# Kernel optimization log

Hardware: AMD Instinct MI355X
Metric: run time of the kernel (lower is better)

## Reference

```python
import jax, jax.numpy as jnp
import numpy as np

N_SP = 32  # number of superpixels, hardcoded in the original module


def setup_inputs() -> dict:
    key = jax.random.key(0)
    k1, k2 = jax.random.split(key)
    b, c, h, w = 16, 64, 512, 512
    features = jax.random.normal(k1, (b, c, h, w), dtype=jnp.float32)
    superpixel_indices = jax.random.randint(k2, (b, h, w), 0, N_SP, dtype=jnp.int32)
    return {"features": features, "superpixel_indices": superpixel_indices}


def reference(features, superpixel_indices):
    b, c, h, w = features.shape
    # [b, h*w, c]
    feats = jnp.transpose(features, (0, 2, 3, 1)).reshape(b * h * w, c)
    # offset segment ids so all batches reduce in one segment_sum pass
    ids = (superpixel_indices.reshape(b, h * w)
           + (jnp.arange(b, dtype=superpixel_indices.dtype)[:, None] * N_SP)).reshape(-1)
    sums = jax.ops.segment_sum(feats, ids, num_segments=b * N_SP)          # [b*N, c]
    counts = jax.ops.segment_sum(jnp.ones((b * h * w,), feats.dtype), ids,
                                 num_segments=b * N_SP)                     # [b*N]
    # mean per superpixel; empty superpixels stay zero (matches torch init)
    sp = jnp.where(counts[:, None] > 0,
                   sums / jnp.maximum(counts[:, None], 1.0),
                   0.0).reshape(b, N_SP, c)
    # pairwise: sim[i,j] = 1 - 0.5 * ||sp_i - sp_j||^2  (N=32, tiny)
    diff = sp[:, :, None, :] - sp[:, None, :, :]        # [b, N, N, c]
    sim = 1.0 - 0.5 * jnp.sum(diff * diff, axis=-1)     # [b, N, N]
    return sp, sim
```

## Files before the change

### kernel.cpp

```cpp
#include <hip/hip_runtime.h>

#define NSP 32
#define BB  16
#define CC  64
#define HH  512
#define WW  512
#define HW  (HH * WW)

#define CHUNK  8192
#define BLOCK  256
#define NCHUNK (HW / CHUNK)

#define CNT_CHUNK 16384

__global__ __launch_bounds__(BLOCK) void sp_accum(const float* __restrict__ feats,
                                                  const int*   __restrict__ spidx,
                                                  float*       __restrict__ sums )
{
    __shared__ unsigned char s_idx[CHUNK];
    __shared__ float2 s_priv[BLOCK][NSP + 1];
    __shared__ float2 s_part[8][NSP];

    const int tid  = threadIdx.x;
    const int b    = blockIdx.y;
    const int pix0 = blockIdx.x * CHUNK;

    const int4* ip = (const int4*)(spidx + (size_t)b * HW + pix0);
    uchar4* sip = (uchar4*)s_idx;
    for (int i = tid; i < CHUNK / 4; i += BLOCK) {
        int4 v = ip[i];
        sip[i] = make_uchar4((unsigned char)(v.x & 31), (unsigned char)(v.y & 31),
                             (unsigned char)(v.z & 31), (unsigned char)(v.w & 31));
    }
#pragma unroll
    for (int sp = 0; sp < NSP; ++sp) s_priv[tid][sp] = make_float2(0.f, 0.f);
    __syncthreads();

    const int bin = tid & 31;
    const int grp = tid >> 5;

    for (int cp = 0; cp < CC; cp += 2) {
        const float4* f0 = (const float4*)(feats + ((size_t)b * CC + cp)     * HW + pix0);
        const float4* f1 = (const float4*)(feats + ((size_t)b * CC + cp + 1) * HW + pix0);
        float2* row = s_priv[tid];

#pragma unroll
        for (int k = 0; k < CHUNK / 4 / BLOCK; ++k) {
            const int i = k * BLOCK + tid;
            float4 a = f0[i];
            float4 c = f1[i];
            uchar4 u = sip[i];
            float2 t;
            t = row[u.x]; t.x += a.x; t.y += c.x; row[u.x] = t;
            t = row[u.y]; t.x += a.y; t.y += c.y; row[u.y] = t;
            t = row[u.z]; t.x += a.z; t.y += c.z; row[u.z] = t;
            t = row[u.w]; t.x += a.w; t.y += c.w; row[u.w] = t;
        }
        __syncthreads();

        float2 acc = make_float2(0.f, 0.f);
#pragma unroll
        for (int m = 0; m < BLOCK / 8; ++m) {
            float2 v = s_priv[grp + m * 8][bin];
            acc.x += v.x; acc.y += v.y;
        }
        s_part[grp][bin] = acc;
        __syncthreads();

        if (cp + 2 < CC) {
#pragma unroll
            for (int sp = 0; sp < NSP; ++sp) s_priv[tid][sp] = make_float2(0.f, 0.f);
        }
        if (tid < NSP) {
            float2 r = s_part[0][tid];
#pragma unroll
            for (int g2 = 1; g2 < 8; ++g2) { r.x += s_part[g2][tid].x; r.y += s_part[g2][tid].y; }
            atomicAdd(&sums[((size_t)b * CC + cp)     * NSP + tid], r.x);
            atomicAdd(&sums[((size_t)b * CC + cp + 1) * NSP + tid], r.y);
        }
        __syncthreads();
    }
}

__global__ __launch_bounds__(BLOCK) void sp_count(const int* __restrict__ spidx,
                                                  float*     __restrict__ counts )
{
    __shared__ int s_cnt[BLOCK][NSP + 1];
    __shared__ int s_tot[NSP];
    const int tid  = threadIdx.x;
    const int b    = blockIdx.y;
    const int pix0 = blockIdx.x * CNT_CHUNK;

#pragma unroll
    for (int sp = 0; sp < NSP; ++sp) s_cnt[tid][sp] = 0;
    if (tid < NSP) s_tot[tid] = 0;
    __syncthreads();

    const int4* ip = (const int4*)(spidx + (size_t)b * HW + pix0);
    int* row = s_cnt[tid];
    for (int i = tid; i < CNT_CHUNK / 4; i += BLOCK) {
        int4 v = ip[i];
        row[v.x & 31]++;
        row[v.y & 31]++;
        row[v.z & 31]++;
        row[v.w & 31]++;
    }
    __syncthreads();

    const int bin = tid & 31, grp = tid >> 5;
    int acc = 0;
#pragma unroll
    for (int m = 0; m < BLOCK / 8; ++m) acc += s_cnt[grp + m * 8][bin];
    atomicAdd(&s_tot[bin], acc);
    __syncthreads();

    if (tid < NSP) atomicAdd(&counts[b * NSP + tid], (float)s_tot[tid]);
}

__global__ __launch_bounds__(BLOCK) void sp_finalize(const float* __restrict__ sums,
                                                     const float* __restrict__ counts,
                                                     float*       __restrict__ out)
{
    __shared__ float s_sp[NSP][CC + 1];
    const int b   = blockIdx.x;
    const int tid = threadIdx.x;

    for (int i = tid; i < NSP * CC; i += BLOCK) {
        int sp = i >> 6, c = i & 63;
        float cnt = counts[b * NSP + sp];
        float s   = sums[((size_t)b * CC + c) * NSP + sp];
        float v   = (cnt > 0.0f) ? (s / cnt) : 0.0f;
        s_sp[sp][c] = v;
        out[(size_t)b * NSP * CC + (size_t)sp * CC + c] = v;
    }
    __syncthreads();

    for (int p = tid; p < NSP * NSP; p += BLOCK) {
        int i = p >> 5, j = p & 31;
        float acc = 0.0f;
#pragma unroll
        for (int c = 0; c < CC; ++c) {
            float d = s_sp[i][c] - s_sp[j][c];
            acc = fmaf(d, d, acc);
        }
        out[(size_t)BB * NSP * CC + (size_t)b * NSP * NSP + p] = 1.0f - 0.5f * acc;
    }
}

extern "C" void kernel_launch(void* const* d_in, const int* in_sizes, int n_in,
                              void* d_out, int out_size, void* d_ws, size_t ws_size,
                              hipStream_t stream)
{
    const float* feats = (const float*)d_in[0];
    const int*   spidx = (const int*)d_in[1];
    float*       out   = (float*)d_out;

    float* sums   = (float*)d_ws;
    float* counts = sums + (size_t)BB * CC * NSP;

    hipMemsetAsync(d_ws, 0, ((size_t)BB * CC * NSP + (size_t)BB * NSP) * sizeof(float), stream);

    dim3 g1(NCHUNK, BB);
    sp_accum<<<g1, BLOCK, 0, stream>>>(feats, spidx, sums);

    dim3 g2(HW / CNT_CHUNK, BB);
    sp_count<<<g2, BLOCK, 0, stream>>>(spidx, counts);

    sp_finalize<<<BB, BLOCK, 0, stream>>>(sums, counts, out);
}
```

Baseline: 224.6 us.

## Fuse count kernel into accumulation and prefetch next channel pair into registers

Removes the separate sp_count kernel and computes per-superpixel counts inside sp_accum from the already-staged index tile, saving one launch and a second read of the index array. The feature loads for the next channel pair are issued into registers before the reduction and barrier phases, so global memory latency overlaps with the shared-memory reduction. __syncthreads is replaced by an inline-asm barrier that waits only on LDS counters, which lets the prefetched global loads stay in flight across barriers. This raises register pressure (16 float4 values held per thread) and depends on the hand-written barrier being correct.

```diff
diff --git a/kernel.cpp b/kernel.cpp
--- a/kernel.cpp
+++ b/kernel.cpp
@@ -3,118 +3,124 @@
 #define NSP 32
 #define BB  16
 #define CC  64
-#define HH  512
-#define WW  512
-#define HW  (HH * WW)
+#define HW  (512 * 512)
 
+#define BLOCK  256
 #define CHUNK  8192
-#define BLOCK  256
 #define NCHUNK (HW / CHUNK)
+#define KIT    (CHUNK / 4 / BLOCK)
 
-#define CNT_CHUNK 16384
+#define BAR() asm volatile("s_waitcnt lgkmcnt(0)\n\ts_barrier" ::: "memory")
 
 __global__ __launch_bounds__(BLOCK) void sp_accum(const float* __restrict__ feats,
                                                   const int*   __restrict__ spidx,
-                                                  float*       __restrict__ sums )
+                                                  float*       __restrict__ sums  ,
+                                                  float*       __restrict__ counts)
 {
-    __shared__ unsigned char s_idx[CHUNK];
+    __shared__ uchar4 s_idx[CHUNK / 4];
     __shared__ float2 s_priv[BLOCK][NSP + 1];
     __shared__ float2 s_part[8][NSP];
 
     const int tid  = threadIdx.x;
     const int b    = blockIdx.y;
     const int pix0 = blockIdx.x * CHUNK;
+    const int bin  = tid & 31;
+    const int grp  = tid >> 5;
 
     const int4* ip = (const int4*)(spidx + (size_t)b * HW + pix0);
-    uchar4* sip = (uchar4*)s_idx;
-    for (int i = tid; i < CHUNK / 4; i += BLOCK) {
+#pragma unroll
+    for (int n = 0; n < (CHUNK / 4) / BLOCK; ++n) {
+        const int i = n * BLOCK + tid;
         int4 v = ip[i];
-        sip[i] = make_uchar4((unsigned char)(v.x & 31), (unsigned char)(v.y & 31),
-                             (unsigned char)(v.z & 31), (unsigned char)(v.w & 31));
+        s_idx[i] = make_uchar4((unsigned char)(v.x & 31), (unsigned char)(v.y & 31),
+                               (unsigned char)(v.z & 31), (unsigned char)(v.w & 31));
     }
 #pragma unroll
     for (int sp = 0; sp < NSP; ++sp) s_priv[tid][sp] = make_float2(0.f, 0.f);
-    __syncthreads();
 
-    const int bin = tid & 31;
-    const int grp = tid >> 5;
+    const float* fb = feats + (size_t)b * CC * HW + pix0;
+    float4 pre[KIT][2];
+#pragma unroll
+    for (int k = 0; k < KIT; ++k) {
+        pre[k][0] = ((const float4*)fb)[k * BLOCK + tid];
+        pre[k][1] = ((const float4*)(fb + (size_t)HW))[k * BLOCK + tid];
+    }
 
-    for (int cp = 0; cp < CC; cp += 2) {
-        const float4* f0 = (const float4*)(feats + ((size_t)b * CC + cp)     * HW + pix0);
-        const float4* f1 = (const float4*)(feats + ((size_t)b * CC + cp + 1) * HW + pix0);
-        float2* row = s_priv[tid];
+    BAR();
 
+    {
+        float* rowf = (float*)&s_priv[tid][0];
 #pragma unroll
-        for (int k = 0; k < CHUNK / 4 / BLOCK; ++k) {
-            const int i = k * BLOCK + tid;
-            float4 a = f0[i];
-            float4 c = f1[i];
-            uchar4 u = sip[i];
+        for (int k = 0; k < KIT; ++k) {
+            uchar4 u = s_idx[k * BLOCK + tid];
+            rowf[u.x * 2] += 1.f;
+            rowf[u.y * 2] += 1.f;
+            rowf[u.z * 2] += 1.f;
+            rowf[u.w * 2] += 1.f;
+        }
+    }
+    BAR();
+    {
+        float a = 0.f;
+#pragma unroll
+        for (int m = 0; m < BLOCK / 8; ++m) a += s_priv[grp + m * 8][bin].x;
+        s_part[grp][bin].x = a;
+    }
+    BAR();
+    if (tid < NSP) {
+        float r = 0.f;
+#pragma unroll
+        for (int g = 0; g < 8; ++g) r += s_part[g][tid].x;
+        atomicAdd(&counts[b * NSP + tid], r);
+    }
+#pragma unroll
+    for (int sp = 0; sp < NSP; ++sp) s_priv[tid][sp] = make_float2(0.f, 0.f);
+    BAR();
+
+    float2* row = s_priv[tid];
+    for (int cp = 0; cp < CC / 2; ++cp) {
+#pragma unroll
+        for (int k = 0; k < KIT; ++k) {
+            uchar4 u = s_idx[k * BLOCK + tid];
+            float4 a = pre[k][0], c = pre[k][1];
             float2 t;
             t = row[u.x]; t.x += a.x; t.y += c.x; row[u.x] = t;
             t = row[u.y]; t.x += a.y; t.y += c.y; row[u.y] = t;
             t = row[u.z]; t.x += a.z; t.y += c.z; row[u.z] = t;
             t = row[u.w]; t.x += a.w; t.y += c.w; row[u.w] = t;
         }
-        __syncthreads();
-
-        float2 acc = make_float2(0.f, 0.f);
+        if (cp + 1 < CC / 2) {
+            const float* g0 = fb + (size_t)(2 * cp + 2) * HW;
 #pragma unroll
-        for (int m = 0; m < BLOCK / 8; ++m) {
-            float2 v = s_priv[grp + m * 8][bin];
-            acc.x += v.x; acc.y += v.y;
+            for (int k = 0; k < KIT; ++k) {
+                pre[k][0] = ((const float4*)g0)[k * BLOCK + tid];
+                pre[k][1] = ((const float4*)(g0 + (size_t)HW))[k * BLOCK + tid];
+            }
         }
-        s_part[grp][bin] = acc;
-        __syncthreads();
-
-        if (cp + 2 < CC) {
+        BAR();
+        {
+            float2 acc = make_float2(0.f, 0.f);
 #pragma unroll
-            for (int sp = 0; sp < NSP; ++sp) s_priv[tid][sp] = make_float2(0.f, 0.f);
+            for (int m = 0; m < BLOCK / 8; ++m) {
+                float2 v = s_priv[grp + m * 8][bin];
+                acc.x += v.x; acc.y += v.y;
+            }
+            s_part[grp][bin] = acc;
+        }
+        BAR();
+        if (cp + 1 < CC / 2) {
+#pragma unroll
+            for (int sp = 0; sp < NSP; ++sp) row[sp] = make_float2(0.f, 0.f);
         }
         if (tid < NSP) {
             float2 r = s_part[0][tid];
 #pragma unroll
-            for (int g2 = 1; g2 < 8; ++g2) { r.x += s_part[g2][tid].x; r.y += s_part[g2][tid].y; }
-            atomicAdd(&sums[((size_t)b * CC + cp)     * NSP + tid], r.x);
-            atomicAdd(&sums[((size_t)b * CC + cp + 1) * NSP + tid], r.y);
+            for (int g = 1; g < 8; ++g) { r.x += s_part[g][tid].x; r.y += s_part[g][tid].y; }
+            atomicAdd(&sums[((size_t)b * CC + 2 * cp)     * NSP + tid], r.x);
+            atomicAdd(&sums[((size_t)b * CC + 2 * cp + 1) * NSP + tid], r.y);
         }
-        __syncthreads();
+        BAR();
     }
-}
-
-__global__ __launch_bounds__(BLOCK) void sp_count(const int* __restrict__ spidx,
-                                                  float*     __restrict__ counts )
-{
-    __shared__ int s_cnt[BLOCK][NSP + 1];
-    __shared__ int s_tot[NSP];
-    const int tid  = threadIdx.x;
-    const int b    = blockIdx.y;
-    const int pix0 = blockIdx.x * CNT_CHUNK;
-
-#pragma unroll
-    for (int sp = 0; sp < NSP; ++sp) s_cnt[tid][sp] = 0;
-    if (tid < NSP) s_tot[tid] = 0;
-    __syncthreads();
-
-    const int4* ip = (const int4*)(spidx + (size_t)b * HW + pix0);
-    int* row = s_cnt[tid];
-    for (int i = tid; i < CNT_CHUNK / 4; i += BLOCK) {
-        int4 v = ip[i];
-        row[v.x & 31]++;
-        row[v.y & 31]++;
-        row[v.z & 31]++;
-        row[v.w & 31]++;
-    }
-    __syncthreads();
-
-    const int bin = tid & 31, grp = tid >> 5;
-    int acc = 0;
-#pragma unroll
-    for (int m = 0; m < BLOCK / 8; ++m) acc += s_cnt[grp + m * 8][bin];
-    atomicAdd(&s_tot[bin], acc);
-    __syncthreads();
-
-    if (tid < NSP) atomicAdd(&counts[b * NSP + tid], (float)s_tot[tid]);
 }
 
 __global__ __launch_bounds__(BLOCK) void sp_finalize(const float* __restrict__ sums,
@@ -161,10 +167,7 @@
     hipMemsetAsync(d_ws, 0, ((size_t)BB * CC * NSP + (size_t)BB * NSP) * sizeof(float), stream);
 
     dim3 g1(NCHUNK, BB);
-    sp_accum<<<g1, BLOCK, 0, stream>>>(feats, spidx, sums);
-
-    dim3 g2(HW / CNT_CHUNK, BB);
-    sp_count<<<g2, BLOCK, 0, stream>>>(spidx, counts);
+    sp_accum<<<g1, BLOCK, 0, stream>>>(feats, spidx, sums, counts);
 
     sp_finalize<<<BB, BLOCK, 0, stream>>>(sums, counts, out);
 }
```

Result: faster. 213.2 us (median of 2 runs) (-5.1%).
